# Kernel optimization log

Hardware: AMD Instinct MI355X
Metric: run time of the kernel (lower is better)

Reference implementation:

```python
import jax, jax.numpy as jnp
import numpy as np

NINP = 512
NHEAD = 8


def setup_inputs() -> dict:
    key = jax.random.key(0)
    ks = jax.random.split(key, 7)
    B, M, L, C = 2, 32, 512, NINP
    s = 1.0 / np.sqrt(C)
    return {
        "x": jax.random.normal(ks[0], (B, M, L, C), dtype=jnp.float32),
        "Wq": jax.random.normal(ks[1], (C, C), dtype=jnp.float32) * s,
        "bq": jax.random.normal(ks[2], (C,), dtype=jnp.float32) * s,
        "Wk": jax.random.normal(ks[3], (C, C), dtype=jnp.float32) * s,
        "bk": jax.random.normal(ks[4], (C,), dtype=jnp.float32) * s,
        "Wv": jax.random.normal(ks[5], (C, C), dtype=jnp.float32) * s,
        "bv": jax.random.normal(ks[6], (C,), dtype=jnp.float32) * s,
    }


def reference(x, Wq, bq, Wk, bk, Wv, bv) -> jnp.ndarray:
    # x: (B, M, L, C). Attention over L within each (B, M) block.
    B, M, L, C = x.shape
    H = NHEAD
    D = C // H
    scale = 1.0 / jnp.sqrt(jnp.asarray(D, dtype=x.dtype))

    def split_heads(t):  # (B,M,L,C) -> (B,M,H,L,D)
        return t.reshape(B, M, L, H, D).transpose(0, 1, 3, 2, 4)

    q = split_heads(x @ Wq + bq)
    k = split_heads(x @ Wk + bk)
    v = split_heads(x @ Wv + bv)

    scores = jnp.einsum("bmhid,bmhjd->bmhij", q, k) * scale
    w = jax.nn.softmax(scores, axis=-1)  # dropout p=0 -> identity
    out = jnp.einsum("bmhij,bmhjd->bmhid", w, v)  # (B,M,H,L,D)
    return out.transpose(0, 1, 3, 2, 4).reshape(B, M, L, C)
```

## Files before the change

kernel.cpp:

```cpp
#include <hip/hip_runtime.h>


typedef unsigned short u16;
typedef unsigned int u32;
typedef unsigned long long u64;
typedef __bf16 bf16x8 __attribute__((ext_vector_type(8)));
typedef float f32x4 __attribute__((ext_vector_type(4)));

#define SCQ 0.18033688011112042f

static __device__ __forceinline__ u16 f2bf(float f) {
  u32 x = __float_as_uint(f);
  x += 0x7fffu + ((x >> 16) & 1u);
  return (u16)(x >> 16);
}

static __device__ __forceinline__ u32 cvtpk(float lo, float hi) {
  u32 r;
  asm("v_cvt_pk_bf16_f32 %0, %1, %2" : "=v"(r) : "v"(lo), "v"(hi));
  return r;
}

typedef __attribute__((address_space(1))) const void* gvp;
typedef __attribute__((address_space(3))) void* lvp;
static __device__ __forceinline__ void glds16(const void* g, void* l) {
  __builtin_amdgcn_global_load_lds((gvp)g, (lvp)l, 16, 0, 0);
}

__global__ __launch_bounds__(256) void prep(const float* __restrict__ x,
                                            u16* __restrict__ xb,
                                            const float* __restrict__ Wq,
                                            const float* __restrict__ Wk,
                                            const float* __restrict__ Wv,
                                            u16* __restrict__ WT) {
  __shared__ float t[32][33];
  const int bx = blockIdx.x;
  if (bx < 8192) {
    const u32 i = (bx * 256u + threadIdx.x) * 8u;
    const float4 a = *(const float4*)(x + i);
    const float4 b = *(const float4*)(x + i + 4);
    union { u16 r[8]; uint4 v; } u;
    u.r[0] = f2bf(a.x); u.r[1] = f2bf(a.y); u.r[2] = f2bf(a.z); u.r[3] = f2bf(a.w);
    u.r[4] = f2bf(b.x); u.r[5] = f2bf(b.y); u.r[6] = f2bf(b.z); u.r[7] = f2bf(b.w);
    *(uint4*)(xb + i) = u.v;
    return;
  }
  const int b = bx - 8192;
  const int z = b >> 8;
  const int rem = b & 255;
  const float* W = (z == 0) ? Wq : ((z == 1) ? Wk : Wv);
  u16* dst = WT + z * 262144;
  const int k0 = (rem >> 4) * 32, n0 = (rem & 15) * 32;
  const int tx = threadIdx.x & 31, ty = threadIdx.x >> 5;
#pragma unroll
  for (int i = 0; i < 32; i += 8)
    t[ty + i][tx] = W[(size_t)(k0 + ty + i) * 512 + n0 + tx];
  __syncthreads();
#pragma unroll
  for (int i = 0; i < 32; i += 8)
    dst[(size_t)(n0 + ty + i) * 512 + k0 + tx] = f2bf(t[tx][ty + i]);
}

__global__ __launch_bounds__(256) void gemm_qkv(const u16* __restrict__ xb,
                                                const u16* __restrict__ WT,
                                                const float* __restrict__ bq,
                                                const float* __restrict__ bk,
                                                const float* __restrict__ bv,
                                                u16* __restrict__ qkv) {
  __shared__ __align__(16) u16 smem[32768];
  const int id = blockIdx.x;
  const int xcd = id & 7;
  const int slot = id >> 3;
  const int r12 = slot % 12;
  const int z = r12 >> 2;
  const int m = (slot / 12) * 8 + xcd;
  const int mbase = m * 128;
  const int nbase = (r12 & 3) * 128;
  const u16* Bg = WT + z * 262144;
  const float* bias = (z == 0) ? bq : ((z == 1) ? bk : bv);
  u16* out = qkv + (size_t)z * 16777216u;
  const int tid = threadIdx.x;
  const int lane = tid & 63;
  const int w = tid >> 6;
  const int wy = w >> 1, wx = w & 1;
  const int m15 = lane & 15, g = lane >> 4;

  const int srow = w * 32 + (lane >> 2);
  const int scol = (lane & 3) * 8;
  const u16* Ap = xb + (size_t)(mbase + srow) * 512 + scol;
  const u16* Bp = Bg + (size_t)(nbase + srow) * 512 + scol;

  f32x4 acc[4][4] = {};

#define STAGE(KT, B)                                  \
  do {                                                \
    const int k0_ = (KT) * 32;                        \
    u16* d_ = (B) + w * 1024;                         \
    glds16(Ap + k0_, d_);                             \
    glds16(Ap + k0_ + 16 * 512, d_ + 512);            \
    glds16(Bp + k0_, d_ + 4096);                      \
    glds16(Bp + k0_ + 16 * 512, d_ + 4096 + 512);     \
  } while (0)

#define COMPUTE(B)                                                          \
  do {                                                                      \
    bf16x8 af[4], bfr[4];                                                   \
    _Pragma("unroll") for (int t = 0; t < 4; ++t)                           \
        af[t] = *(const bf16x8*)&(B)[(wy * 64 + t * 16 + m15) * 32 + g * 8];\
    _Pragma("unroll") for (int t = 0; t < 4; ++t)                           \
        bfr[t] = *(const bf16x8*)&(B)[4096 + (wx * 64 + t * 16 + m15) * 32 + g * 8]; \
    _Pragma("unroll") for (int rt = 0; rt < 4; ++rt)                        \
        _Pragma("unroll") for (int ct = 0; ct < 4; ++ct)                    \
            acc[rt][ct] = __builtin_amdgcn_mfma_f32_16x16x32_bf16(          \
                af[rt], bfr[ct], acc[rt][ct], 0, 0, 0);                     \
  } while (0)

  STAGE(0, smem);
  STAGE(1, smem + 8192);
  STAGE(2, smem + 16384);

#pragma unroll
  for (int kt = 0; kt < 16; ++kt) {
    u16* cb = smem + (kt & 3) * 8192;
    if (kt < 14)
      asm volatile("s_waitcnt vmcnt(8)" ::: "memory");
    else if (kt == 14)
      asm volatile("s_waitcnt vmcnt(4)" ::: "memory");
    else
      asm volatile("s_waitcnt vmcnt(0)" ::: "memory");
    __builtin_amdgcn_s_barrier();
    if (kt + 3 < 16) STAGE(kt + 3, smem + ((kt + 3) & 3) * 8192);
    COMPUTE(cb);
    asm volatile("s_waitcnt lgkmcnt(0)" ::: "memory");
  }
#undef STAGE
#undef COMPUTE

  if (z < 2) {
    const float sc = (z == 0) ? SCQ : 1.0f;
#pragma unroll
    for (int ct = 0; ct < 4; ++ct) {
      const int col = nbase + wx * 64 + ct * 16 + m15;
      const float bb = bias[col];
#pragma unroll
      for (int rt = 0; rt < 4; ++rt) {
        const int row0 = mbase + wy * 64 + rt * 16 + g * 4;
#pragma unroll
        for (int r = 0; r < 4; ++r)
          out[(size_t)(row0 + r) * 512 + col] = f2bf((acc[rt][ct][r] + bb) * sc);
      }
    }
  } else {
    const int bm = mbase >> 9, jb = mbase & 511;
    u16* sT = smem;
#pragma unroll
    for (int cn = 0; cn < 4; ++cn) {
      __syncthreads();
      if (wx == (cn >> 1)) {
#pragma unroll
        for (int cte = 0; cte < 2; ++cte) {
          const int ct = (cn & 1) * 2 + cte;
          const int ncol = nbase + wx * 64 + ct * 16 + m15;
          const float bb = bias[ncol];
          const int nl = cte * 16 + m15;
#pragma unroll
          for (int rt = 0; rt < 4; ++rt) {
            u64 pk = 0;
#pragma unroll
            for (int r = 0; r < 4; ++r)
              pk |= (u64)f2bf(acc[rt][ct][r] + bb) << (16 * r);
            *(u64*)&sT[nl * 136 + wy * 64 + rt * 16 + g * 4] = pk;
          }
        }
      }
      __syncthreads();
#pragma unroll
      for (int it = 0; it < 2; ++it) {
        const int nl = it * 16 + (tid >> 4);
        const int ml = (tid & 15) * 8;
        const int ng = nbase + cn * 32 + nl;
        const int h = ng >> 6, d = ng & 63;
        *(uint4*)(out + ((size_t)((bm * 8 + h) * 64 + d)) * 512 + jb + ml) =
            *(const uint4*)&sT[nl * 136 + ml];
      }
    }
  }
}

__global__ __launch_bounds__(256) void attn(const u16* __restrict__ Q,
                                            const u16* __restrict__ K,
                                            const u16* __restrict__ Vt,
                                            float* __restrict__ out) {
  __shared__ __align__(16) char smem[36864];
  u16* sK = (u16*)smem;
  u16* sVT = (u16*)(smem + 9216);
  const int tid = threadIdx.x;
  const int lane = tid & 63;
  const int w = tid >> 6;
  const int m15 = lane & 15, g = lane >> 4;
  const int id = blockIdx.x;
  const int h = id & 7;
  const int bm = id >> 5;
  const int qt = (id >> 3) & 3;
  const size_t rb = (size_t)bm * 512;
  const int q0 = qt * 128 + w * 32;
  u16* sPT = (u16*)(smem + 18432) + w * 2304;

  bf16x8 qf[2][2];
#pragma unroll
  for (int ct = 0; ct < 2; ++ct)
#pragma unroll
    for (int kc = 0; kc < 2; ++kc)
      qf[ct][kc] =
          *(const bf16x8*)(Q + (rb + q0 + ct * 16 + m15) * 512 + h * 64 + kc * 32 + g * 8);

  bf16x8 ones;
#pragma unroll
  for (int i = 0; i < 8; ++i) ones[i] = (__bf16)1.0f;

  f32x4 acc[4][2] = {};
  f32x4 accL[2] = {};

  const int srow = tid >> 3, sc8 = (tid & 7) * 8;
  const u16* Kb = K + rb * 512 + h * 64;
  const u16* Vtb = Vt + (size_t)(bm * 8 + h) * 64 * 512;

  uint4 k0v = *(const uint4*)(Kb + (size_t)srow * 512 + sc8);
  uint4 k1v = *(const uint4*)(Kb + (size_t)(srow + 32) * 512 + sc8);
  uint4 v0v = *(const uint4*)(Vtb + (size_t)srow * 512 + sc8);
  uint4 v1v = *(const uint4*)(Vtb + (size_t)(srow + 32) * 512 + sc8);

  for (int jt = 0; jt < 8; ++jt) {
    asm volatile("s_waitcnt lgkmcnt(0)" ::: "memory");
    __builtin_amdgcn_s_barrier();
    asm volatile("s_waitcnt vmcnt(0)" ::: "memory");
    *(uint4*)&sK[srow * 72 + sc8] = k0v;
    *(uint4*)&sK[(srow + 32) * 72 + sc8] = k1v;
    *(uint4*)&sVT[srow * 72 + sc8] = v0v;
    *(uint4*)&sVT[(srow + 32) * 72 + sc8] = v1v;
    if (jt < 7) {
      const int j1 = (jt + 1) * 64;
      k0v = *(const uint4*)(Kb + (size_t)(j1 + srow) * 512 + sc8);
      k1v = *(const uint4*)(Kb + (size_t)(j1 + srow + 32) * 512 + sc8);
      v0v = *(const uint4*)(Vtb + (size_t)srow * 512 + j1 + sc8);
      v1v = *(const uint4*)(Vtb + (size_t)(srow + 32) * 512 + j1 + sc8);
    }
    asm volatile("s_waitcnt lgkmcnt(0)" ::: "memory");
    __builtin_amdgcn_s_barrier();

    f32x4 s[4][2];
#pragma unroll
    for (int rt = 0; rt < 4; ++rt) {
      const bf16x8 k0 = *(const bf16x8*)&sK[(rt * 16 + m15) * 72 + g * 8];
      const bf16x8 k1 = *(const bf16x8*)&sK[(rt * 16 + m15) * 72 + 32 + g * 8];
#pragma unroll
      for (int ct = 0; ct < 2; ++ct) {
        f32x4 z = {};
        z = __builtin_amdgcn_mfma_f32_16x16x32_bf16(k0, qf[ct][0], z, 0, 0, 0);
        s[rt][ct] = __builtin_amdgcn_mfma_f32_16x16x32_bf16(k1, qf[ct][1], z, 0, 0, 0);
      }
    }

#pragma unroll
    for (int ct = 0; ct < 2; ++ct)
#pragma unroll
      for (int rt = 0; rt < 4; ++rt) {
        f32x4 p;
#pragma unroll
        for (int r = 0; r < 4; ++r) p[r] = exp2f(s[rt][ct][r]);
        uint2 pk = {cvtpk(p[0], p[1]), cvtpk(p[2], p[3])};
        *(uint2*)&sPT[(ct * 16 + m15) * 72 + rt * 16 + g * 4] = pk;
      }

    bf16x8 pb[2][2];
#pragma unroll
    for (int ct = 0; ct < 2; ++ct)
#pragma unroll
      for (int kc = 0; kc < 2; ++kc)
        pb[ct][kc] = *(const bf16x8*)&sPT[(ct * 16 + m15) * 72 + kc * 32 + g * 8];
#pragma unroll
    for (int ct = 0; ct < 2; ++ct) {
      accL[ct] = __builtin_amdgcn_mfma_f32_16x16x32_bf16(ones, pb[ct][0], accL[ct], 0, 0, 0);
      accL[ct] = __builtin_amdgcn_mfma_f32_16x16x32_bf16(ones, pb[ct][1], accL[ct], 0, 0, 0);
    }
#pragma unroll
    for (int dt = 0; dt < 4; ++dt) {
      const bf16x8 v0 = *(const bf16x8*)&sVT[(dt * 16 + m15) * 72 + g * 8];
      const bf16x8 v1 = *(const bf16x8*)&sVT[(dt * 16 + m15) * 72 + 32 + g * 8];
#pragma unroll
      for (int ct = 0; ct < 2; ++ct) {
        acc[dt][ct] = __builtin_amdgcn_mfma_f32_16x16x32_bf16(v0, pb[ct][0], acc[dt][ct], 0, 0, 0);
        acc[dt][ct] = __builtin_amdgcn_mfma_f32_16x16x32_bf16(v1, pb[ct][1], acc[dt][ct], 0, 0, 0);
      }
    }
  }

  float inv[2];
#pragma unroll
  for (int ct = 0; ct < 2; ++ct) inv[ct] = 1.0f / accL[ct][0];
  __syncthreads();
  float* sO = (float*)(smem + w * 4608);
#pragma unroll
  for (int c = 0; c < 2; ++c) {
#pragma unroll
    for (int dt2 = 0; dt2 < 2; ++dt2)
#pragma unroll
      for (int ct = 0; ct < 2; ++ct) {
        f32x4 v = acc[c * 2 + dt2][ct] * inv[ct];
        *(f32x4*)&sO[(ct * 16 + m15) * 36 + dt2 * 16 + g * 4] = v;
      }
#pragma unroll
    for (int it = 0; it < 4; ++it) {
      const int q = it * 8 + (lane >> 3);
      f32x4 v = *(const f32x4*)&sO[q * 36 + (lane & 7) * 4];
      *(f32x4*)&out[(rb + q0 + q) * 512 + h * 64 + c * 32 + (lane & 7) * 4] = v;
    }
  }
}

extern "C" void kernel_launch(void* const* d_in, const int* in_sizes, int n_in,
                              void* d_out, int out_size, void* d_ws, size_t ws_size,
                              hipStream_t stream) {
  const float* x = (const float*)d_in[0];
  const float* Wq = (const float*)d_in[1];
  const float* bq = (const float*)d_in[2];
  const float* Wk = (const float*)d_in[3];
  const float* bk = (const float*)d_in[4];
  const float* Wv = (const float*)d_in[5];
  const float* bv = (const float*)d_in[6];
  float* out = (float*)d_out;

  u16* ws = (u16*)d_ws;
  u16* xb = ws;
  u16* WT = ws + 16777216;
  u16* qkv = ws + 17563648;

  prep<<<8960, 256, 0, stream>>>(x, xb, Wq, Wk, Wv, WT);
  gemm_qkv<<<3072, 256, 0, stream>>>(xb, WT, bq, bk, bv, qkv);
  attn<<<2048, 256, 0, stream>>>(qkv, qkv + 16777216, qkv + 2 * 16777216, out);
}
```

Measured before the change: 250.8 us.

## Widen QKV GEMM tile to 128x256 with triple-buffered LDS pipeline

Each QKV GEMM block now computes a 128x256 output tile instead of 128x128, which halves the grid and doubles the accumulators per wave (4x8 MFMA tiles). Each A tile is reused across twice as many columns, so redundant global loads of x drop. LDS staging moves from four buffers to three, with a second barrier before each refill. The cost is higher register pressure, possibly lower occupancy, and an extra barrier per k-step.

```diff
diff --git a/kernel.cpp b/kernel.cpp
--- a/kernel.cpp
+++ b/kernel.cpp
@@ -67,15 +67,15 @@
                                                 const float* __restrict__ bk,
                                                 const float* __restrict__ bv,
                                                 u16* __restrict__ qkv) {
-  __shared__ __align__(16) u16 smem[32768];
+  __shared__ __align__(16) u16 smem[36864];
   const int id = blockIdx.x;
   const int xcd = id & 7;
   const int slot = id >> 3;
-  const int r12 = slot % 12;
-  const int z = r12 >> 2;
-  const int m = (slot / 12) * 8 + xcd;
+  const int zn = slot % 6;
+  const int m = (slot / 6) * 8 + xcd;
   const int mbase = m * 128;
-  const int nbase = (r12 & 3) * 128;
+  const int z = zn >> 1;
+  const int nbase = (zn & 1) * 256;
   const u16* Bg = WT + z * 262144;
   const float* bias = (z == 0) ? bq : ((z == 1) ? bk : bv);
   u16* out = qkv + (size_t)z * 16777216u;
@@ -85,53 +85,57 @@
   const int wy = w >> 1, wx = w & 1;
   const int m15 = lane & 15, g = lane >> 4;
 
-  const int srow = w * 32 + (lane >> 2);
+  const int lrow = lane >> 2;
   const int scol = (lane & 3) * 8;
-  const u16* Ap = xb + (size_t)(mbase + srow) * 512 + scol;
-  const u16* Bp = Bg + (size_t)(nbase + srow) * 512 + scol;
-
-  f32x4 acc[4][4] = {};
-
-#define STAGE(KT, B)                                  \
-  do {                                                \
-    const int k0_ = (KT) * 32;                        \
-    u16* d_ = (B) + w * 1024;                         \
-    glds16(Ap + k0_, d_);                             \
-    glds16(Ap + k0_ + 16 * 512, d_ + 512);            \
-    glds16(Bp + k0_, d_ + 4096);                      \
-    glds16(Bp + k0_ + 16 * 512, d_ + 4096 + 512);     \
+  const u16* Ap = xb + (size_t)(mbase + w * 32 + lrow) * 512 + scol;
+  const u16* Bp = Bg + (size_t)(nbase + w * 64 + lrow) * 512 + scol;
+
+  f32x4 acc[4][8] = {};
+
+#define STAGE(KT, B)                                   \
+  do {                                                 \
+    const int k0_ = (KT) * 32;                         \
+    u16* da_ = (B) + w * 1024;                         \
+    glds16(Ap + k0_, da_);                             \
+    glds16(Ap + k0_ + 16 * 512, da_ + 512);            \
+    u16* db_ = (B) + 4096 + w * 2048;                  \
+    glds16(Bp + k0_, db_);                             \
+    glds16(Bp + k0_ + 16 * 512, db_ + 512);            \
+    glds16(Bp + k0_ + 32 * 512, db_ + 1024);           \
+    glds16(Bp + k0_ + 48 * 512, db_ + 1536);           \
   } while (0)
 
 #define COMPUTE(B)                                                          \
   do {                                                                      \
-    bf16x8 af[4], bfr[4];                                                   \
+    bf16x8 af[4], bfr[8];                                                   \
     _Pragma("unroll") for (int t = 0; t < 4; ++t)                           \
         af[t] = *(const bf16x8*)&(B)[(wy * 64 + t * 16 + m15) * 32 + g * 8];\
-    _Pragma("unroll") for (int t = 0; t < 4; ++t)                           \
-        bfr[t] = *(const bf16x8*)&(B)[4096 + (wx * 64 + t * 16 + m15) * 32 + g * 8]; \
+    _Pragma("unroll") for (int t = 0; t < 8; ++t)                           \
+        bfr[t] = *(const bf16x8*)&(B)[4096 + (wx * 128 + t * 16 + m15) * 32 + g * 8]; \
     _Pragma("unroll") for (int rt = 0; rt < 4; ++rt)                        \
-        _Pragma("unroll") for (int ct = 0; ct < 4; ++ct)                    \
+        _Pragma("unroll") for (int ct = 0; ct < 8; ++ct)                    \
             acc[rt][ct] = __builtin_amdgcn_mfma_f32_16x16x32_bf16(          \
                 af[rt], bfr[ct], acc[rt][ct], 0, 0, 0);                     \
   } while (0)
 
   STAGE(0, smem);
-  STAGE(1, smem + 8192);
-  STAGE(2, smem + 16384);
+  STAGE(1, smem + 12288);
+  STAGE(2, smem + 24576);
 
 #pragma unroll
   for (int kt = 0; kt < 16; ++kt) {
-    u16* cb = smem + (kt & 3) * 8192;
+    u16* cb = smem + (kt % 3) * 12288;
     if (kt < 14)
-      asm volatile("s_waitcnt vmcnt(8)" ::: "memory");
+      asm volatile("s_waitcnt vmcnt(12)" ::: "memory");
     else if (kt == 14)
-      asm volatile("s_waitcnt vmcnt(4)" ::: "memory");
+      asm volatile("s_waitcnt vmcnt(6)" ::: "memory");
     else
       asm volatile("s_waitcnt vmcnt(0)" ::: "memory");
     __builtin_amdgcn_s_barrier();
-    if (kt + 3 < 16) STAGE(kt + 3, smem + ((kt + 3) & 3) * 8192);
     COMPUTE(cb);
     asm volatile("s_waitcnt lgkmcnt(0)" ::: "memory");
+    __builtin_amdgcn_s_barrier();
+    if (kt + 3 < 16) STAGE(kt + 3, cb);
   }
 #undef STAGE
 #undef COMPUTE
@@ -139,8 +143,8 @@
   if (z < 2) {
     const float sc = (z == 0) ? SCQ : 1.0f;
 #pragma unroll
-    for (int ct = 0; ct < 4; ++ct) {
-      const int col = nbase + wx * 64 + ct * 16 + m15;
+    for (int ct = 0; ct < 8; ++ct) {
+      const int col = nbase + wx * 128 + ct * 16 + m15;
       const float bb = bias[col];
 #pragma unroll
       for (int rt = 0; rt < 4; ++rt) {
@@ -154,13 +158,13 @@
     const int bm = mbase >> 9, jb = mbase & 511;
     u16* sT = smem;
 #pragma unroll
-    for (int cn = 0; cn < 4; ++cn) {
+    for (int cn = 0; cn < 8; ++cn) {
       __syncthreads();
-      if (wx == (cn >> 1)) {
+      if (wx == (cn >> 2)) {
 #pragma unroll
         for (int cte = 0; cte < 2; ++cte) {
-          const int ct = (cn & 1) * 2 + cte;
-          const int ncol = nbase + wx * 64 + ct * 16 + m15;
+          const int ct = (cn & 3) * 2 + cte;
+          const int ncol = nbase + wx * 128 + ct * 16 + m15;
           const float bb = bias[ncol];
           const int nl = cte * 16 + m15;
 #pragma unroll
@@ -336,6 +340,6 @@
   u16* qkv = ws + 17563648;
 
   prep<<<8960, 256, 0, stream>>>(x, xb, Wq, Wk, Wv, WT);
-  gemm_qkv<<<3072, 256, 0, stream>>>(xb, WT, bq, bk, bv, qkv);
+  gemm_qkv<<<1536, 256, 0, stream>>>(xb, WT, bq, bk, bv, qkv);
   attn<<<2048, 256, 0, stream>>>(qkv, qkv + 16777216, qkv + 2 * 16777216, out);
 }
```

Result: slower. 265.8 us (+6.0%).
